# Performance work log

Hardware: AMD Instinct MI355X
Metric: run time of the kernel (lower is better)

The kernel has to match this reference:

```python
import jax, jax.numpy as jnp
import numpy as np

D_MODEL = 1024
NUM_HEADS = 16
THETA = 10000.0


def _rope(x, cos, sin):
    # x: [B, H, S, dk]; cos/sin: [B, 1, S, dk//2]
    x1 = x[..., 0::2]
    x2 = x[..., 1::2]
    r1 = x1 * cos - x2 * sin
    r2 = x1 * sin + x2 * cos
    return jnp.stack([r1, r2], axis=-1).reshape(x.shape)


def setup_inputs() -> dict:
    key = jax.random.key(0)
    ks = jax.random.split(key, 5)
    B, S, D = 2, 2048, D_MODEL
    std = np.sqrt(2.0 / (D + D))
    x = jax.random.normal(ks[0], (B, S, D), dtype=jnp.float32)
    Wq = jax.random.normal(ks[1], (D, D), dtype=jnp.float32) * std
    Wk = jax.random.normal(ks[2], (D, D), dtype=jnp.float32) * std
    Wv = jax.random.normal(ks[3], (D, D), dtype=jnp.float32) * std
    Wo = jax.random.normal(ks[4], (D, D), dtype=jnp.float32) * std
    token_positions = jnp.broadcast_to(jnp.arange(S, dtype=jnp.int32), (B, S))
    return {"x": x, "Wq": Wq, "Wk": Wk, "Wv": Wv, "Wo": Wo,
            "token_positions": token_positions}


def reference(x, Wq, Wk, Wv, Wo, token_positions):
    B, S, D = x.shape
    H = NUM_HEADS
    dk = D // H

    def split_heads(t):  # [B,S,D] -> [B,H,S,dk]
        return t.reshape(B, S, H, dk).transpose(0, 2, 1, 3)

    Q = split_heads(x @ Wq)
    K = split_heads(x @ Wk)
    V = split_heads(x @ Wv)

    # RoPE angles: theta^(-2i/dk) frequencies, indexed by token positions
    freqs = THETA ** (-jnp.arange(0, dk, 2, dtype=jnp.float32) / dk)  # [dk/2]
    angles = token_positions.astype(jnp.float32)[..., None] * freqs   # [B,S,dk/2]
    cos = jnp.cos(angles)[:, None]  # [B,1,S,dk/2] broadcast over heads
    sin = jnp.sin(angles)[:, None]
    Q = _rope(Q, cos, sin)
    K = _rope(K, cos, sin)

    scores = jnp.einsum('bhqd,bhkd->bhqk', Q, K) / jnp.sqrt(jnp.float32(dk))
    causal = jnp.tril(jnp.ones((S, S), dtype=bool))  # [S,S]
    scores = jnp.where(causal[None, None], scores, -jnp.inf)
    probs = jax.nn.softmax(scores, axis=-1)
    att = jnp.einsum('bhqk,bhkd->bhqd', probs, V)  # [B,H,S,dk]
    att = att.transpose(0, 2, 1, 3).reshape(B, S, D)
    return att @ Wo
```

## Files before the change

### kernel.cpp

```cpp
#include <hip/hip_runtime.h>
#include <math.h>

#define SLEN 2048
#define DMODEL 1024
#define NHEADS 16
#define DK 64
#define NBATCH 2
#define M_TOT (NBATCH * SLEN)
#define NQKV (3 * DMODEL)

typedef __bf16 bf16x8 __attribute__((ext_vector_type(8)));
typedef float f32x4 __attribute__((ext_vector_type(4)));
typedef float f32x16 __attribute__((ext_vector_type(16)));

static __device__ __forceinline__ unsigned short f2bf(float f) {
    unsigned int u = __float_as_uint(f);
    u += 0x7fffu + ((u >> 16) & 1u);
    return (unsigned short)(u >> 16);
}

static __device__ __forceinline__ unsigned cvtpk(float a, float b) {
    unsigned r;
    asm("v_cvt_pk_bf16_f32 %0, %1, %2" : "=v"(r) : "v"(a), "v"(b));
    return r;
}

#if __has_builtin(__builtin_amdgcn_exp2f)
#define EXP2(x) __builtin_amdgcn_exp2f(x)
#else
#define EXP2(x) exp2f(x)
#endif

static __device__ __forceinline__ void gload16(const void* g, void* l) {
    __builtin_amdgcn_global_load_lds(
        (const __attribute__((address_space(1))) unsigned int*)g,
        (__attribute__((address_space(3))) unsigned int*)l, 16, 0, 0);
}

__global__ __launch_bounds__(256)
void convert_bf16(const float* __restrict__ X, unsigned short* __restrict__ Xb, int n4)
{
    int i = blockIdx.x * 256 + threadIdx.x;
    if (i < n4) {
        float4 v = *(const float4*)&X[(size_t)i * 4];
        ushort4 o;
        o.x = f2bf(v.x); o.y = f2bf(v.y); o.z = f2bf(v.z); o.w = f2bf(v.w);
        *(ushort4*)&Xb[(size_t)i * 4] = o;
    }
}

__global__ __launch_bounds__(256)
void transpose_w(const float* __restrict__ W, unsigned short* __restrict__ Wt)
{
    __shared__ float t[64][65];
    const int tid = threadIdx.x;
    const int c0 = blockIdx.x * 64, r0 = blockIdx.y * 64;
    const int tr = tid >> 4, tc = (tid & 15) * 4;
    #pragma unroll
    for (int rr = 0; rr < 4; ++rr) {
        int row = rr * 16 + tr;
        float4 v = *(const float4*)&W[(size_t)(r0 + row) * DMODEL + c0 + tc];
        t[row][tc + 0] = v.x; t[row][tc + 1] = v.y;
        t[row][tc + 2] = v.z; t[row][tc + 3] = v.w;
    }
    __syncthreads();
    #pragma unroll
    for (int rr = 0; rr < 4; ++rr) {
        int orow = rr * 16 + tr;
        ushort4 o;
        o.x = f2bf(t[tc + 0][orow]);
        o.y = f2bf(t[tc + 1][orow]);
        o.z = f2bf(t[tc + 2][orow]);
        o.w = f2bf(t[tc + 3][orow]);
        *(ushort4*)&Wt[(size_t)(c0 + orow) * DMODEL + r0 + tc] = o;
    }
}

template<int MODE>
__global__ __launch_bounds__(256)
void gemm_mfma(const unsigned short* __restrict__ A,
               const unsigned short* __restrict__ Bt,
               float* __restrict__ C,
               unsigned short* __restrict__ Qd,
               unsigned short* __restrict__ Kd,
               unsigned short* __restrict__ Vtd,
               const int* __restrict__ pos,
               int N, int K)
{
    __shared__ unsigned short AB[2 * 2 * 128 * 64];
    const int tid = threadIdx.x;
    const int w = tid >> 6, l = tid & 63;
    const int m0 = blockIdx.y * 128, n0 = blockIdx.x * 128;
    const int wr = (w >> 1) * 64, wc = (w & 1) * 64;
    const int lr = l >> 3, lp = l & 7;

    f32x4 acc[4][4] = {};

    auto STAGE = [&](int k0, int buf) {
        unsigned short* Asd = AB + buf * (2 * 128 * 64);
        unsigned short* Bsd = Asd + 128 * 64;
        #pragma unroll
        for (int i = 0; i < 4; ++i) {
            int row = w * 32 + i * 8 + lr;
            int s = lp ^ (row & 7);
            gload16(A  + (size_t)(m0 + row) * K + k0 + s * 8, (void*)(Asd + (w * 32 + i * 8) * 64));
            gload16(Bt + (size_t)(n0 + row) * K + k0 + s * 8, (void*)(Bsd + (w * 32 + i * 8) * 64));
        }
    };

    const int nt = K >> 6;
    STAGE(0, 0);

    for (int t = 0; t < nt; ++t) {
        __syncthreads();
        if (t + 1 < nt) STAGE((t + 1) << 6, (t + 1) & 1);
        const char* Asb = (const char*)AB + (t & 1) * 32768;
        const char* Bsb = Asb + 16384;
        #pragma unroll
        for (int ks = 0; ks < 2; ++ks) {
            bf16x8 af[4], bfr[4];
            #pragma unroll
            for (int i = 0; i < 4; ++i) {
                int row = wr + i * 16 + (l & 15);
                int slot = (ks * 4 + (l >> 4)) ^ (row & 7);
                af[i] = *(const bf16x8*)(Asb + row * 128 + slot * 16);
            }
            #pragma unroll
            for (int j = 0; j < 4; ++j) {
                int row = wc + j * 16 + (l & 15);
                int slot = (ks * 4 + (l >> 4)) ^ (row & 7);
                bfr[j] = *(const bf16x8*)(Bsb + row * 128 + slot * 16);
            }
            __builtin_amdgcn_s_setprio(1);
            #pragma unroll
            for (int i = 0; i < 4; ++i)
                #pragma unroll
                for (int j = 0; j < 4; ++j)
                    acc[i][j] = __builtin_amdgcn_mfma_f32_16x16x32_bf16(af[i], bfr[j], acc[i][j], 0, 0, 0);
            __builtin_amdgcn_s_setprio(0);
        }
    }

    if (MODE == 0) {
        #pragma unroll
        for (int i = 0; i < 4; ++i)
            #pragma unroll
            for (int j = 0; j < 4; ++j)
                #pragma unroll
                for (int r = 0; r < 4; ++r) {
                    int row = m0 + wr + i * 16 + (l >> 4) * 4 + r;
                    int col = n0 + wc + j * 16 + (l & 15);
                    C[(size_t)row * N + col] = acc[i][j][r];
                }
    } else {
        const int seg = (n0 + wc) >> 10;
        #pragma unroll
        for (int i = 0; i < 4; ++i) {
            const int mbase = m0 + wr + i * 16 + (l >> 4) * 4;
            #pragma unroll
            for (int j = 0; j < 4; ++j) {
                const int n = n0 + wc + j * 16 + (l & 15);
                const int h = (n >> 6) & 15;
                const int d = n & 63;
                if (seg < 2) {
                    unsigned short* dst = (seg == 0) ? Qd : Kd;
                    const int de = d & ~1;
                    const float freq = __expf((float)de * (-9.210340371976184f / 64.f));
                    #pragma unroll
                    for (int r = 0; r < 4; ++r) {
                        const int m = mbase + r;
                        const int b = m >> 11, s = m & 2047;
                        float v = acc[i][j][r];
                        float p2 = __shfl_xor(v, 1);
                        float ang = (float)pos[m] * freq;
                        float sn, cs;
                        __sincosf(ang, &sn, &cs);
                        float res = ((l & 1) == 0) ? (v * cs - p2 * sn) : (p2 * sn + v * cs);
                        if (seg == 0) res *= 0.18033688011112042f;
                        dst[((size_t)(b * NHEADS + h) * SLEN + s) * DK + d] = f2bf(res);
                    }
                } else {
                    const int b = mbase >> 11, s0 = mbase & 2047;
                    const int tile = s0 >> 5, ksv = (s0 >> 4) & 1, hb = (s0 >> 3) & 1, j0 = s0 & 7;
                    const int mt2v = d >> 5, c31v = d & 31;
                    size_t idx = (size_t)(b * NHEADS + h) * 131072 + tile * 2048
                               + ksv * 1024 + mt2v * 512 + hb * 256 + c31v * 8 + j0;
                    ushort4 o;
                    o.x = f2bf(acc[i][j][0]); o.y = f2bf(acc[i][j][1]);
                    o.z = f2bf(acc[i][j][2]); o.w = f2bf(acc[i][j][3]);
                    *(ushort4*)&Vtd[idx] = o;
                }
            }
        }
    }
}

__global__ __launch_bounds__(128)
void attn_mfma(const unsigned short* __restrict__ Q,
               const unsigned short* __restrict__ K,
               const unsigned short* __restrict__ Vf,
               unsigned short* __restrict__ Oa)
{
    __shared__ char smem[17408];
    const int tid = threadIdx.x;
    const int w = tid >> 6, l = tid & 63;
    const int h = l >> 5, c31 = l & 31;

    const int id = blockIdx.x;
    const int bh = (id & 7) * 4 + ((id >> 3) & 3);
    const int g  = 63 - (id >> 5);
    const int n_w = (g >= w) ? ((g - w) >> 1) + 1 : 0;

    const unsigned short* Qb  = Q  + (size_t)bh * SLEN * DK;
    const unsigned short* Kb  = K  + (size_t)bh * SLEN * DK;
    const unsigned short* VfB = Vf + (size_t)bh * 131072;

    const int q_g = g * 32 + c31;

    bf16x8 qf[4];
    #pragma unroll
    for (int kb = 0; kb < 4; ++kb)
        qf[kb] = *(const bf16x8*)(Qb + (size_t)q_g * DK + kb * 16 + h * 8);

    float m = -1e30f, lsum = 0.f;
    f32x16 oacc[2] = {};

    char* mybuf = smem + w * 8192;
    auto STAGE = [&](int t, int p) {
        char* dst = mybuf + p * 4096;
        const unsigned short* src = Kb + (size_t)t * 2048;
        #pragma unroll
        for (int i2 = 0; i2 < 4; ++i2) {
            int row = i2 * 8 + (l >> 3);
            gload16(src + row * 64 + (((l & 7) ^ (row & 7)) * 8), dst + i2 * 1024);
        }
    };

    if (n_w > 0) {
        STAGE(w, 0);
        if (n_w > 1) STAGE(w + 2, 1);

        for (int i = 0; i < n_w; ++i) {
            const int t = w + 2 * i;
            const bool last = (i == n_w - 1);
            if (last) { asm volatile("s_waitcnt vmcnt(0)" ::: "memory"); }
            else      { asm volatile("s_waitcnt vmcnt(4)" ::: "memory"); }
            __builtin_amdgcn_sched_barrier(0);

            bf16x8 vf0, vf1, vf2, vf3;
            {
                const unsigned short* vsrc = VfB + (size_t)t * 2048 + l * 8;
                vf0 = *(const bf16x8*)(vsrc);
                vf1 = *(const bf16x8*)(vsrc + 512);
                vf2 = *(const bf16x8*)(vsrc + 1024);
                vf3 = *(const bf16x8*)(vsrc + 1536);
            }

            const char* kbuf = mybuf + (i & 1) * 4096;
            f32x16 sacc = {};
            __builtin_amdgcn_s_setprio(1);
            #pragma unroll
            for (int kb = 0; kb < 4; ++kb) {
                bf16x8 kf = *(const bf16x8*)(kbuf + c31 * 128 + ((((kb * 2 + h)) ^ (c31 & 7)) << 4));
                sacc = __builtin_amdgcn_mfma_f32_32x32x16_bf16(kf, qf[kb], sacc, 0, 0, 0);
            }
            __builtin_amdgcn_s_setprio(0);

            if (last && w == (g & 1)) {
                #pragma unroll
                for (int r = 0; r < 16; ++r) {
                    int crow = (r & 3) + 8 * (r >> 2) + 4 * h;
                    if (crow > c31) sacc[r] = -1e30f;
                }
            }

            float t16[16];
            #pragma unroll
            for (int r = 0; r < 16; ++r) t16[r] = sacc[r];
            #pragma unroll
            for (int s = 8; s > 0; s >>= 1)
                #pragma unroll
                for (int r = 0; r < s; ++r) t16[r] = fmaxf(t16[r], t16[r + s]);
            float mx = t16[0];
            mx = fmaxf(mx, __shfl_xor(mx, 32));

            if (mx > m + 6.0f) {
                float corr = EXP2(m - mx);
                m = mx;
                lsum *= corr;
                oacc[0] *= corr;
                oacc[1] *= corr;
            }

            float ps = 0.f;
            #pragma unroll
            for (int r = 0; r < 16; ++r) {
                float e = EXP2(sacc[r] - m);
                sacc[r] = e;
                ps += e;
            }
            lsum += ps;

            #pragma unroll
            for (int ks = 0; ks < 2; ++ks) {
                const int rb = ks * 8;
                unsigned pk0 = cvtpk(sacc[rb + 0], sacc[rb + 1]);
                unsigned pk1 = cvtpk(sacc[rb + 2], sacc[rb + 3]);
                unsigned pk2 = cvtpk(sacc[rb + 4], sacc[rb + 5]);
                unsigned pk3 = cvtpk(sacc[rb + 6], sacc[rb + 7]);
                unsigned s0 = (unsigned)__shfl_xor((int)pk0, 32);
                unsigned s1 = (unsigned)__shfl_xor((int)pk1, 32);
                unsigned s2 = (unsigned)__shfl_xor((int)pk2, 32);
                unsigned s3 = (unsigned)__shfl_xor((int)pk3, 32);
                union { unsigned u[4]; bf16x8 v; } pf;
                pf.u[0] = (h == 0) ? pk0 : s2;
                pf.u[1] = (h == 0) ? pk1 : s3;
                pf.u[2] = (h == 0) ? s0 : pk2;
                pf.u[3] = (h == 0) ? s1 : pk3;
                __builtin_amdgcn_s_setprio(1);
                oacc[0] = __builtin_amdgcn_mfma_f32_32x32x16_bf16(ks ? vf2 : vf0, pf.v, oacc[0], 0, 0, 0);
                oacc[1] = __builtin_amdgcn_mfma_f32_32x32x16_bf16(ks ? vf3 : vf1, pf.v, oacc[1], 0, 0, 0);
                __builtin_amdgcn_s_setprio(0);
            }

            if (i + 2 < n_w) STAGE(w + 2 * (i + 2), i & 1);
        }
    }

    __syncthreads();
    float* Lm = (float*)(smem + 16384);
    float* Ll = (float*)(smem + 16384 + 256);
    if (h == 0) Lm[w * 32 + c31] = m;
    Ll[(w * 2 + h) * 32 + c31] = lsum;
    __syncthreads();
    const float m0 = Lm[c31], m1 = Lm[32 + c31];
    const float mstar = fmaxf(m0, m1);
    const float s_w = EXP2(m - mstar);
    const float lstar = EXP2(m0 - mstar) * (Ll[c31] + Ll[32 + c31])
                      + EXP2(m1 - mstar) * (Ll[64 + c31] + Ll[96 + c31]);

    float* Op = (float*)smem;
    if (w == 0) {
        #pragma unroll
        for (int mt = 0; mt < 2; ++mt)
            #pragma unroll
            for (int r = 0; r < 16; ++r)
                Op[(mt * 16 + r) * 64 + l] = oacc[mt][r] * s_w;
    }
    __syncthreads();
    if (w == 1) {
        const float inv = 1.f / lstar;
        unsigned short* Os = (unsigned short*)(smem + 8192);
        #pragma unroll
        for (int mt = 0; mt < 2; ++mt)
            #pragma unroll
            for (int rq = 0; rq < 4; ++rq) {
                float a0 = (Op[(mt * 16 + rq * 4 + 0) * 64 + l] + oacc[mt][rq * 4 + 0] * s_w) * inv;
                float a1 = (Op[(mt * 16 + rq * 4 + 1) * 64 + l] + oacc[mt][rq * 4 + 1] * s_w) * inv;
                float a2 = (Op[(mt * 16 + rq * 4 + 2) * 64 + l] + oacc[mt][rq * 4 + 2] * s_w) * inv;
                float a3 = (Op[(mt * 16 + rq * 4 + 3) * 64 + l] + oacc[mt][rq * 4 + 3] * s_w) * inv;
                uint2 pv;
                pv.x = cvtpk(a0, a1);
                pv.y = cvtpk(a2, a3);
                int dbyte = mt * 64 + rq * 16 + h * 8;
                *(uint2*)((char*)Os + c31 * 128 + (dbyte ^ ((c31 & 7) << 4))) = pv;
            }
        const int b = bh >> 4, hh = bh & 15;
        const int cc = l & 7;
        #pragma unroll
        for (int pp = 0; pp < 4; ++pp) {
            int row = pp * 8 + (l >> 3);
            uint4 vv = *(const uint4*)((const char*)Os + row * 128 + ((cc ^ (row & 7)) << 4));
            int srow = g * 32 + row;
            *(uint4*)&Oa[((size_t)(b * SLEN + srow)) * DMODEL + hh * DK + cc * 8] = vv;
        }
    }
}

extern "C" void kernel_launch(void* const* d_in, const int* in_sizes, int n_in,
                              void* d_out, int out_size, void* d_ws, size_t ws_size,
                              hipStream_t stream)
{
    const float* x  = (const float*)d_in[0];
    const float* Wq = (const float*)d_in[1];
    const float* Wk = (const float*)d_in[2];
    const float* Wv = (const float*)d_in[3];
    const float* Wo = (const float*)d_in[4];
    const int*  pos = (const int*)d_in[5];
    float* out = (float*)d_out;

    char* ws = (char*)d_ws;
    const size_t MB = 1024 * 1024;
    unsigned short* xb   = (unsigned short*)(ws);
    unsigned short* Wcat = (unsigned short*)(ws + 8 * MB);
    unsigned short* Wot  = (unsigned short*)(ws + 14 * MB);
    unsigned short* Qws  = (unsigned short*)(ws + 16 * MB);
    unsigned short* Kws  = (unsigned short*)(ws + 24 * MB);
    unsigned short* Vfws = (unsigned short*)(ws + 32 * MB);
    unsigned short* attb = (unsigned short*)(ws + 40 * MB);

    convert_bf16<<<4096, 256, 0, stream>>>(x, xb, M_TOT * DMODEL / 4);
    transpose_w<<<dim3(16, 16), 256, 0, stream>>>(Wq, Wcat);
    transpose_w<<<dim3(16, 16), 256, 0, stream>>>(Wk, Wcat + 1024 * 1024);
    transpose_w<<<dim3(16, 16), 256, 0, stream>>>(Wv, Wcat + 2 * 1024 * 1024);
    transpose_w<<<dim3(16, 16), 256, 0, stream>>>(Wo, Wot);

    gemm_mfma<1><<<dim3(NQKV / 128, M_TOT / 128), 256, 0, stream>>>(
        xb, Wcat, nullptr, Qws, Kws, Vfws, pos, NQKV, DMODEL);

    attn_mfma<<<2048, 128, 0, stream>>>(Qws, Kws, Vfws, attb);

    gemm_mfma<0><<<dim3(DMODEL / 128, M_TOT / 128), 256, 0, stream>>>(
        attb, Wot, out, nullptr, nullptr, nullptr, nullptr, DMODEL, DMODEL);
}
```

Measured before the change: 122.7 us.

## Store K in MFMA fragment layout, drop LDS staging, precompute RoPE table

The QKV GEMM epilogue now writes K directly in the per-lane MFMA fragment order, as was already done for V. This lets the attention kernel load K fragments straight from global memory into registers and drops the async LDS staging, its double buffer and waitcnt logic. LDS use shrinks and launch bounds request 4 blocks per SM. A separate small kernel precomputes the RoPE cos/sin table, so the GEMM epilogue no longer evaluates exp and sincos per element. The trade-offs are losing prefetch overlap of K loads in the attention loop, an extra kernel launch, and scattered 2-byte stores in the K epilogue.

```diff
diff --git a/kernel.cpp b/kernel.cpp
--- a/kernel.cpp
+++ b/kernel.cpp
@@ -47,6 +47,18 @@
         o.x = f2bf(v.x); o.y = f2bf(v.y); o.z = f2bf(v.z); o.w = f2bf(v.w);
         *(ushort4*)&Xb[(size_t)i * 4] = o;
     }
+}
+
+__global__ __launch_bounds__(256)
+void rope_tab(const int* __restrict__ pos, float2* __restrict__ tab)
+{
+    int i = blockIdx.x * 256 + threadIdx.x;
+    int m = i >> 5, de2 = i & 31;
+    float freq = __expf((float)(de2 * 2) * (-9.210340371976184f / 64.f));
+    float ang = (float)pos[m] * freq;
+    float sn, cs;
+    __sincosf(ang, &sn, &cs);
+    tab[i] = make_float2(cs, sn);
 }
 
 __global__ __launch_bounds__(256)
@@ -84,7 +96,7 @@
                unsigned short* __restrict__ Qd,
                unsigned short* __restrict__ Kd,
                unsigned short* __restrict__ Vtd,
-               const int* __restrict__ pos,
+               const float2* __restrict__ tab,
                int N, int K)
 {
     __shared__ unsigned short AB[2 * 2 * 128 * 64];
@@ -164,20 +176,26 @@
                 const int d = n & 63;
                 if (seg < 2) {
                     unsigned short* dst = (seg == 0) ? Qd : Kd;
-                    const int de = d & ~1;
-                    const float freq = __expf((float)de * (-9.210340371976184f / 64.f));
+                    const int de2 = d >> 1;
+                    const int kb = d >> 4, h2 = (d >> 3) & 1, j0 = d & 7;
                     #pragma unroll
                     for (int r = 0; r < 4; ++r) {
-                        const int m = mbase + r;
-                        const int b = m >> 11, s = m & 2047;
+                        const int mm = mbase + r;
+                        const int b = mm >> 11, s = mm & 2047;
                         float v = acc[i][j][r];
                         float p2 = __shfl_xor(v, 1);
-                        float ang = (float)pos[m] * freq;
-                        float sn, cs;
-                        __sincosf(ang, &sn, &cs);
-                        float res = ((l & 1) == 0) ? (v * cs - p2 * sn) : (p2 * sn + v * cs);
-                        if (seg == 0) res *= 0.18033688011112042f;
-                        dst[((size_t)(b * NHEADS + h) * SLEN + s) * DK + d] = f2bf(res);
+                        float2 cssn = tab[mm * 32 + de2];
+                        float res = ((l & 1) == 0) ? (v * cssn.x - p2 * cssn.y)
+                                                   : (p2 * cssn.y + v * cssn.x);
+                        if (seg == 0) {
+                            res *= 0.18033688011112042f;
+                            dst[((size_t)(b * NHEADS + h) * SLEN + s) * DK + d] = f2bf(res);
+                        } else {
+                            size_t idx = (size_t)(b * NHEADS + h) * 131072
+                                       + (size_t)(s >> 5) * 2048 + kb * 512 + h2 * 256
+                                       + (s & 31) * 8 + j0;
+                            dst[idx] = f2bf(res);
+                        }
                     }
                 } else {
                     const int b = mbase >> 11, s0 = mbase & 2047;
@@ -195,13 +213,13 @@
     }
 }
 
-__global__ __launch_bounds__(128)
+__global__ __launch_bounds__(128, 4)
 void attn_mfma(const unsigned short* __restrict__ Q,
-               const unsigned short* __restrict__ K,
+               const unsigned short* __restrict__ Kf,
                const unsigned short* __restrict__ Vf,
                unsigned short* __restrict__ Oa)
 {
-    __shared__ char smem[17408];
+    __shared__ char smem[13056];
     const int tid = threadIdx.x;
     const int w = tid >> 6, l = tid & 63;
     const int h = l >> 5, c31 = l & 31;
@@ -212,8 +230,8 @@
     const int n_w = (g >= w) ? ((g - w) >> 1) + 1 : 0;
 
     const unsigned short* Qb  = Q  + (size_t)bh * SLEN * DK;
-    const unsigned short* Kb  = K  + (size_t)bh * SLEN * DK;
-    const unsigned short* VfB = Vf + (size_t)bh * 131072;
+    const unsigned short* KfB = Kf + (size_t)bh * 131072 + l * 8;
+    const unsigned short* VfB = Vf + (size_t)bh * 131072 + l * 8;
 
     const int q_g = g * 32 + c31;
 
@@ -225,111 +243,90 @@
     float m = -1e30f, lsum = 0.f;
     f32x16 oacc[2] = {};
 
-    char* mybuf = smem + w * 8192;
-    auto STAGE = [&](int t, int p) {
-        char* dst = mybuf + p * 4096;
-        const unsigned short* src = Kb + (size_t)t * 2048;
-        #pragma unroll
-        for (int i2 = 0; i2 < 4; ++i2) {
-            int row = i2 * 8 + (l >> 3);
-            gload16(src + row * 64 + (((l & 7) ^ (row & 7)) * 8), dst + i2 * 1024);
-        }
-    };
-
-    if (n_w > 0) {
-        STAGE(w, 0);
-        if (n_w > 1) STAGE(w + 2, 1);
-
-        for (int i = 0; i < n_w; ++i) {
-            const int t = w + 2 * i;
-            const bool last = (i == n_w - 1);
-            if (last) { asm volatile("s_waitcnt vmcnt(0)" ::: "memory"); }
-            else      { asm volatile("s_waitcnt vmcnt(4)" ::: "memory"); }
-            __builtin_amdgcn_sched_barrier(0);
-
-            bf16x8 vf0, vf1, vf2, vf3;
-            {
-                const unsigned short* vsrc = VfB + (size_t)t * 2048 + l * 8;
-                vf0 = *(const bf16x8*)(vsrc);
-                vf1 = *(const bf16x8*)(vsrc + 512);
-                vf2 = *(const bf16x8*)(vsrc + 1024);
-                vf3 = *(const bf16x8*)(vsrc + 1536);
+    for (int i = 0; i < n_w; ++i) {
+        const int t = w + 2 * i;
+        const bool last = (i == n_w - 1);
+        const unsigned short* kp = KfB + (size_t)t * 2048;
+        const unsigned short* vp = VfB + (size_t)t * 2048;
+
+        bf16x8 kf0 = *(const bf16x8*)(kp);
+        bf16x8 kf1 = *(const bf16x8*)(kp + 512);
+        bf16x8 kf2 = *(const bf16x8*)(kp + 1024);
+        bf16x8 kf3 = *(const bf16x8*)(kp + 1536);
+        bf16x8 vf0 = *(const bf16x8*)(vp);
+        bf16x8 vf1 = *(const bf16x8*)(vp + 512);
+        bf16x8 vf2 = *(const bf16x8*)(vp + 1024);
+        bf16x8 vf3 = *(const bf16x8*)(vp + 1536);
+
+        f32x16 sacc = {};
+        __builtin_amdgcn_s_setprio(1);
+        sacc = __builtin_amdgcn_mfma_f32_32x32x16_bf16(kf0, qf[0], sacc, 0, 0, 0);
+        sacc = __builtin_amdgcn_mfma_f32_32x32x16_bf16(kf1, qf[1], sacc, 0, 0, 0);
+        sacc = __builtin_amdgcn_mfma_f32_32x32x16_bf16(kf2, qf[2], sacc, 0, 0, 0);
+        sacc = __builtin_amdgcn_mfma_f32_32x32x16_bf16(kf3, qf[3], sacc, 0, 0, 0);
+        __builtin_amdgcn_s_setprio(0);
+
+        if (last && w == (g & 1)) {
+            #pragma unroll
+            for (int r = 0; r < 16; ++r) {
+                int crow = (r & 3) + 8 * (r >> 2) + 4 * h;
+                if (crow > c31) sacc[r] = -1e30f;
             }
-
-            const char* kbuf = mybuf + (i & 1) * 4096;
-            f32x16 sacc = {};
+        }
+
+        float t16[16];
+        #pragma unroll
+        for (int r = 0; r < 16; ++r) t16[r] = sacc[r];
+        #pragma unroll
+        for (int s = 8; s > 0; s >>= 1)
+            #pragma unroll
+            for (int r = 0; r < s; ++r) t16[r] = fmaxf(t16[r], t16[r + s]);
+        float mx = t16[0];
+        mx = fmaxf(mx, __shfl_xor(mx, 32));
+
+        if (mx > m + 6.0f) {
+            float corr = EXP2(m - mx);
+            m = mx;
+            lsum *= corr;
+            oacc[0] *= corr;
+            oacc[1] *= corr;
+        }
+
+        float ps = 0.f;
+        #pragma unroll
+        for (int r = 0; r < 16; ++r) {
+            float e = EXP2(sacc[r] - m);
+            sacc[r] = e;
+            ps += e;
+        }
+        lsum += ps;
+
+        #pragma unroll
+        for (int ks = 0; ks < 2; ++ks) {
+            const int rb = ks * 8;
+            unsigned pk0 = cvtpk(sacc[rb + 0], sacc[rb + 1]);
+            unsigned pk1 = cvtpk(sacc[rb + 2], sacc[rb + 3]);
+            unsigned pk2 = cvtpk(sacc[rb + 4], sacc[rb + 5]);
+            unsigned pk3 = cvtpk(sacc[rb + 6], sacc[rb + 7]);
+            unsigned s0 = (unsigned)__shfl_xor((int)pk0, 32);
+            unsigned s1 = (unsigned)__shfl_xor((int)pk1, 32);
+            unsigned s2 = (unsigned)__shfl_xor((int)pk2, 32);
+            unsigned s3 = (unsigned)__shfl_xor((int)pk3, 32);
+            union { unsigned u[4]; bf16x8 v; } pf;
+            pf.u[0] = (h == 0) ? pk0 : s2;
+            pf.u[1] = (h == 0) ? pk1 : s3;
+            pf.u[2] = (h == 0) ? s0 : pk2;
+            pf.u[3] = (h == 0) ? s1 : pk3;
             __builtin_amdgcn_s_setprio(1);
-            #pragma unroll
-            for (int kb = 0; kb < 4; ++kb) {
-                bf16x8 kf = *(const bf16x8*)(kbuf + c31 * 128 + ((((kb * 2 + h)) ^ (c31 & 7)) << 4));
-                sacc = __builtin_amdgcn_mfma_f32_32x32x16_bf16(kf, qf[kb], sacc, 0, 0, 0);
-            }
+            oacc[0] = __builtin_amdgcn_mfma_f32_32x32x16_bf16(ks ? vf2 : vf0, pf.v, oacc[0], 0, 0, 0);
+            oacc[1] = __builtin_amdgcn_mfma_f32_32x32x16_bf16(ks ? vf3 : vf1, pf.v, oacc[1], 0, 0, 0);
             __builtin_amdgcn_s_setprio(0);
-
-            if (last && w == (g & 1)) {
-                #pragma unroll
-                for (int r = 0; r < 16; ++r) {
-                    int crow = (r & 3) + 8 * (r >> 2) + 4 * h;
-                    if (crow > c31) sacc[r] = -1e30f;
-                }
-            }
-
-            float t16[16];
-            #pragma unroll
-            for (int r = 0; r < 16; ++r) t16[r] = sacc[r];
-            #pragma unroll
-            for (int s = 8; s > 0; s >>= 1)
-                #pragma unroll
-                for (int r = 0; r < s; ++r) t16[r] = fmaxf(t16[r], t16[r + s]);
-            float mx = t16[0];
-            mx = fmaxf(mx, __shfl_xor(mx, 32));
-
-            if (mx > m + 6.0f) {
-                float corr = EXP2(m - mx);
-                m = mx;
-                lsum *= corr;
-                oacc[0] *= corr;
-                oacc[1] *= corr;
-            }
-
-            float ps = 0.f;
-            #pragma unroll
-            for (int r = 0; r < 16; ++r) {
-                float e = EXP2(sacc[r] - m);
-                sacc[r] = e;
-                ps += e;
-            }
-            lsum += ps;
-
-            #pragma unroll
-            for (int ks = 0; ks < 2; ++ks) {
-                const int rb = ks * 8;
-                unsigned pk0 = cvtpk(sacc[rb + 0], sacc[rb + 1]);
-                unsigned pk1 = cvtpk(sacc[rb + 2], sacc[rb + 3]);
-                unsigned pk2 = cvtpk(sacc[rb + 4], sacc[rb + 5]);
-                unsigned pk3 = cvtpk(sacc[rb + 6], sacc[rb + 7]);
-                unsigned s0 = (unsigned)__shfl_xor((int)pk0, 32);
-                unsigned s1 = (unsigned)__shfl_xor((int)pk1, 32);
-                unsigned s2 = (unsigned)__shfl_xor((int)pk2, 32);
-                unsigned s3 = (unsigned)__shfl_xor((int)pk3, 32);
-                union { unsigned u[4]; bf16x8 v; } pf;
-                pf.u[0] = (h == 0) ? pk0 : s2;
-                pf.u[1] = (h == 0) ? pk1 : s3;
-                pf.u[2] = (h == 0) ? s0 : pk2;
-                pf.u[3] = (h == 0) ? s1 : pk3;
-                __builtin_amdgcn_s_setprio(1);
-                oacc[0] = __builtin_amdgcn_mfma_f32_32x32x16_bf16(ks ? vf2 : vf0, pf.v, oacc[0], 0, 0, 0);
-                oacc[1] = __builtin_amdgcn_mfma_f32_32x32x16_bf16(ks ? vf3 : vf1, pf.v, oacc[1], 0, 0, 0);
-                __builtin_amdgcn_s_setprio(0);
-            }
-
-            if (i + 2 < n_w) STAGE(w + 2 * (i + 2), i & 1);
         }
     }
 
     __syncthreads();
-    float* Lm = (float*)(smem + 16384);
-    float* Ll = (float*)(smem + 16384 + 256);
+    float* Lm = (float*)(smem + 12288);
+    float* Ll = (float*)(smem + 12544);
     if (h == 0) Lm[w * 32 + c31] = m;
     Ll[(w * 2 + h) * 32 + c31] = lsum;
     __syncthreads();
@@ -395,20 +392,22 @@
     unsigned short* Wcat = (unsigned short*)(ws + 8 * MB);
     unsigned short* Wot  = (unsigned short*)(ws + 14 * MB);
     unsigned short* Qws  = (unsigned short*)(ws + 16 * MB);
-    unsigned short* Kws  = (unsigned short*)(ws + 24 * MB);
+    unsigned short* Kfws = (unsigned short*)(ws + 24 * MB);
     unsigned short* Vfws = (unsigned short*)(ws + 32 * MB);
     unsigned short* attb = (unsigned short*)(ws + 40 * MB);
+    float2*         tab  = (float2*)(ws + 48 * MB);
 
     convert_bf16<<<4096, 256, 0, stream>>>(x, xb, M_TOT * DMODEL / 4);
+    rope_tab<<<512, 256, 0, stream>>>(pos, tab);
     transpose_w<<<dim3(16, 16), 256, 0, stream>>>(Wq, Wcat);
     transpose_w<<<dim3(16, 16), 256, 0, stream>>>(Wk, Wcat + 1024 * 1024);
     transpose_w<<<dim3(16, 16), 256, 0, stream>>>(Wv, Wcat + 2 * 1024 * 1024);
     transpose_w<<<dim3(16, 16), 256, 0, stream>>>(Wo, Wot);
 
     gemm_mfma<1><<<dim3(NQKV / 128, M_TOT / 128), 256, 0, stream>>>(
-        xb, Wcat, nullptr, Qws, Kws, Vfws, pos, NQKV, DMODEL);
-
-    attn_mfma<<<2048, 128, 0, stream>>>(Qws, Kws, Vfws, attb);
+        xb, Wcat, nullptr, Qws, Kfws, Vfws, tab, NQKV, DMODEL);
+
+    attn_mfma<<<2048, 128, 0, stream>>>(Qws, Kfws, Vfws, attb);
 
     gemm_mfma<0><<<dim3(DMODEL / 128, M_TOT / 128), 256, 0, stream>>>(
         attb, Wot, out, nullptr, nullptr, nullptr, nullptr, DMODEL, DMODEL);
```

Result: slower. 154.0 us (+25.5%).
